# Kernel tuning notes

Hardware: AMD Instinct MI355X
Metric: run time of the kernel (lower is better)

Reference implementation:

```python
import jax, jax.numpy as jnp
import numpy as np

B, T_PLUS_2, H, K = 128, 2050, 64, 100
BETA = 1.0


def setup_inputs() -> dict:
    key = jax.random.key(0)
    ks = jax.random.split(key, 7)
    event_tensor = jax.random.randint(ks[0], (B, T_PLUS_2), 0, K)            # fine event types
    dtime_tensor = jax.random.uniform(ks[1], (B, T_PLUS_2), dtype=jnp.float32)
    scale = 1.0 / np.sqrt(H)
    in_emb = jax.random.normal(ks[2], (K + 3, H), dtype=jnp.float32) * scale  # +BOS/EOS/PAD rows
    Wx = jax.random.normal(ks[3], (H, 7 * H), dtype=jnp.float32) * scale      # input -> 7 gates
    Wh = jax.random.normal(ks[4], (H, 7 * H), dtype=jnp.float32) * scale      # hidden -> 7 gates
    b = jnp.zeros((7 * H,), dtype=jnp.float32)
    out_emb = jax.random.normal(ks[5], (K, H), dtype=jnp.float32) * scale     # coarse-type embeddings
    return {"event_tensor": event_tensor, "dtime_tensor": dtime_tensor,
            "in_emb": in_emb, "Wx": Wx, "Wh": Wh, "b": b, "out_emb": out_emb}


def _ctlstm_intensities(event_tensor, dtime_tensor, in_emb, Wx, Wh, b, out_emb):
    # Embed input events for steps 0..T (drop last token): [B, T+1, H]
    emb = in_emb[event_tensor[:, :-1]]
    # Precompute the input-dependent part of all 7 gates outside the scan.
    pre = jnp.einsum('bth,hg->btg', emb, Wx) + b        # [B, T+1, 7H]
    dt = dtime_tensor[:, 1:]                            # [B, T+1] dtime to next event

    batch = event_tensor.shape[0]
    h_dim = in_emb.shape[1]
    init = (jnp.zeros((batch, h_dim), jnp.float32),     # c(t_i-)
            jnp.zeros((batch, h_dim), jnp.float32),     # cell_bar
            jnp.zeros((batch, h_dim), jnp.float32))     # h(t_i-)

    def step(carry, inp):
        c_minus, cb_prev, h_minus = carry
        pre_t, dt_t = inp                               # [B,7H], [B]
        g = pre_t + h_minus @ Wh
        gi, gf, gz, go, gib, gfb, gd = jnp.split(g, 7, axis=-1)
        i = jax.nn.sigmoid(gi)
        f = jax.nn.sigmoid(gf)
        z = jnp.tanh(gz)
        o = jax.nn.sigmoid(go)
        i_bar = jax.nn.sigmoid(gib)
        f_bar = jax.nn.sigmoid(gfb)
        delta = jax.nn.softplus(gd)
        c_i = f * c_minus + i * z
        cb_i = f_bar * cb_prev + i_bar * z
        # decay over the interval dt: c(t)=cb+(c-cb)exp(-delta dt), h=o*tanh(c)
        c_next = cb_i + (c_i - cb_i) * jnp.exp(-delta * dt_t[:, None])
        h_next = o * jnp.tanh(c_next)
        return (c_next, cb_i, h_next), h_next

    _, hs = jax.lax.scan(step, init, (pre.transpose(1, 0, 2), dt.T))
    hs = hs.transpose(1, 0, 2)                          # [B, T+1, H] hidden at t_{i+1}^-
    # softplus with beta: (1/beta) * softplus(beta * x); identity fine<->coarse map
    logits = jnp.einsum('bth,kh->btk', hs, out_emb)
    return jax.nn.softplus(BETA * logits) / BETA        # [B, T+1, K]


def reference(event_tensor, dtime_tensor, in_emb, Wx, Wh, b, out_emb):
    return _ctlstm_intensities(event_tensor, dtime_tensor, in_emb, Wx, Wh, b, out_emb)
```

## Files before the change

kernel.cpp:

```cpp
#include <hip/hip_runtime.h>
#include <math.h>

#define BB 128
#define T2 2050
#define TT 2049
#define HH 64
#define GG 448
#define KK 100
#define NE 103

#define LOG2E 1.44269504088896340736f
#define LN2   0.69314718055994530942f

typedef short bf16x8 __attribute__((ext_vector_type(8)));
typedef float f32x4  __attribute__((ext_vector_type(4)));

__device__ __forceinline__ float frcp(float x) { return __builtin_amdgcn_rcpf(x); }

__device__ __forceinline__ float sigmoid_fast(float x) {
    return frcp(1.f + exp2f(-x * LOG2E));
}
__device__ __forceinline__ float tanh_fast(float x) {
    float e = exp2f(x * (2.f * LOG2E));
    return 1.f - 2.f * frcp(1.f + e);
}
__device__ __forceinline__ float softplus_fast(float x) {
    float t = exp2f(-fabsf(x) * LOG2E);
    return fmaxf(x, 0.f) + LN2 * log2f(1.f + t);
}

__device__ __forceinline__ unsigned short bf16_rne(float f) {
    unsigned int u = __builtin_bit_cast(unsigned int, f);
    unsigned int r = u + 0x7FFFu + ((u >> 16) & 1u);
    return (unsigned short)(r >> 16);
}
__device__ __forceinline__ float bf16_to_f(unsigned short s) {
    unsigned int u = ((unsigned int)s) << 16;
    return __builtin_bit_cast(float, u);
}

__global__ void pre_emb_kernel(const float* __restrict__ in_emb,
                               const float* __restrict__ Wx,
                               const float* __restrict__ bias,
                               float* __restrict__ pre_emb) {
    int e = blockIdx.x;
    int t = threadIdx.x;
    float acc = bias[t];
#pragma unroll
    for (int k = 0; k < HH; ++k)
        acc = fmaf(in_emb[e * HH + k], Wx[k * GG + t], acc);
    pre_emb[e * GG + t] = acc;
}

__device__ __forceinline__ void step_barrier() {
    __builtin_amdgcn_sched_barrier(0);
    asm volatile("s_waitcnt lgkmcnt(0)" ::: "memory");
    __builtin_amdgcn_s_barrier();
    __builtin_amdgcn_sched_barrier(0);
}

__launch_bounds__(512, 1)
__global__ void scan_kernel(const int* __restrict__ event,
                            const float* __restrict__ dtime,
                            const float* __restrict__ pre_emb,
                            const float* __restrict__ Wh,
                            const float* __restrict__ oe,
                            float* __restrict__ out) {
    const int b   = blockIdx.x;
    const int tid = threadIdx.x;
    const int w   = tid >> 6;
    const int l   = tid & 63;
    const int q   = l >> 4;
    const int m   = l & 15;

    __shared__ __align__(16) unsigned short hs_hi[2][HH];
    __shared__ __align__(16) unsigned short hs_lo[2][HH];

    const bool is_mat = (w < 4);
    const int  e      = ((w & 3) << 4) | m;

    const int*   ev_row  = event + b * T2;
    const float* dt_row  = dtime + b * T2;
    float*       out_row = out + (size_t)b * TT * KK;

    const f32x4 Z = { 0.f, 0.f, 0.f, 0.f };

    bf16x8 Bhi[7][2], Blo[7][2];
    bf16x8 Phi[2][2], Plo[2][2];
    const int jw  = w - 4;
    const int G0  = 2 * jw;
    const bool has1 = (2 * jw + 1) < 7;
    const int G1  = has1 ? (2 * jw + 1) : G0;

    if (is_mat) {
#pragma unroll
        for (int g = 0; g < 7; ++g) {
#pragma unroll
            for (int kh = 0; kh < 2; ++kh) {
                const int col = g * 64 + e;
                bf16x8 bh, bl;
#pragma unroll
                for (int j = 0; j < 8; ++j) {
                    const int k = kh * 32 + q * 8 + j;
                    const float v = Wh[k * GG + col];
                    const unsigned short hi = bf16_rne(v);
                    bh[j] = (short)hi;
                    bl[j] = (short)bf16_rne(v - bf16_to_f(hi));
                }
                Bhi[g][kh] = bh;
                Blo[g][kh] = bl;
            }
        }
    } else {
#pragma unroll
        for (int s = 0; s < 2; ++s) {
            const int Gs  = s ? G1 : G0;
            int col = Gs * 16 + m;
            if (col > KK - 1) col = KK - 1;
#pragma unroll
            for (int kh = 0; kh < 2; ++kh) {
                bf16x8 bh, bl;
#pragma unroll
                for (int j = 0; j < 8; ++j) {
                    const int k = kh * 32 + q * 8 + j;
                    const float v = oe[col * HH + k];
                    const unsigned short hi = bf16_rne(v);
                    bh[j] = (short)hi;
                    bl[j] = (short)bf16_rne(v - bf16_to_f(hi));
                }
                Phi[s][kh] = bh;
                Plo[s][kh] = bl;
            }
        }
    }

    float pre_cur[7];
    int   evn    = 0;
    float dt_cur = 0.f;
    float c = 0.f, cb = 0.f;
    if (is_mat) {
        const int ev0 = __builtin_amdgcn_readfirstlane(ev_row[0]);
        const float* pb0 = pre_emb + ev0 * GG;
#pragma unroll
        for (int g = 0; g < 7; ++g) pre_cur[g] = pb0[g * 64 + e];
        evn    = __builtin_amdgcn_readfirstlane(ev_row[1]);
        dt_cur = dt_row[1];
    }

    if (tid < HH) { hs_hi[0][tid] = 0; hs_lo[0][tid] = 0; }
    __syncthreads();

    constexpr int GORD[7] = { 6, 2, 0, 1, 4, 5, 3 };

    for (int t = 0; t < TT; ++t) {
        const int rb = t & 1;
        if (is_mat) {
            const float* pb = pre_emb + evn * GG;
            float pre_nxt[7];
#pragma unroll
            for (int g = 0; g < 7; ++g) pre_nxt[g] = pb[g * 64 + e];
            int t2 = t + 2; if (t2 > T2 - 1) t2 = T2 - 1;
            const int   ev_new = __builtin_amdgcn_readfirstlane(ev_row[t2]);
            const float dt_nxt = dt_row[t2];

            const bf16x8 Ahi0 = *(const bf16x8*)&hs_hi[rb][q * 8];
            const bf16x8 Ahi1 = *(const bf16x8*)&hs_hi[rb][32 + q * 8];
            const bf16x8 Alo0 = *(const bf16x8*)&hs_lo[rb][q * 8];
            const bf16x8 Alo1 = *(const bf16x8*)&hs_lo[rb][32 + q * 8];

            float gate[7];
#pragma unroll
            for (int gg = 0; gg < 7; ++gg) {
                const int g = GORD[gg];
                f32x4 aP = __builtin_amdgcn_mfma_f32_16x16x32_bf16(Ahi0, Bhi[g][0], Z, 0, 0, 0);
                f32x4 aQ = __builtin_amdgcn_mfma_f32_16x16x32_bf16(Ahi1, Bhi[g][1], Z, 0, 0, 0);
                aP = __builtin_amdgcn_mfma_f32_16x16x32_bf16(Alo0, Bhi[g][0], aP, 0, 0, 0);
                aQ = __builtin_amdgcn_mfma_f32_16x16x32_bf16(Alo1, Bhi[g][1], aQ, 0, 0, 0);
                aP = __builtin_amdgcn_mfma_f32_16x16x32_bf16(Ahi0, Blo[g][0], aP, 0, 0, 0);
                aQ = __builtin_amdgcn_mfma_f32_16x16x32_bf16(Ahi1, Blo[g][1], aQ, 0, 0, 0);
                gate[g] = pre_cur[g] + (aP[0] + aQ[0]);
            }

            const float ed   = exp2f(-dt_cur * log2f(1.f + exp2f(gate[6] * LOG2E)));
            const float z_g  = tanh_fast(gate[2]);
            const float i_g  = sigmoid_fast(gate[0]);
            const float f_g  = sigmoid_fast(gate[1]);
            const float ib_g = sigmoid_fast(gate[4]);
            const float fb_g = sigmoid_fast(gate[5]);
            const float o_g  = sigmoid_fast(gate[3]);

            const float ci  = fmaf(f_g, c, i_g * z_g);
            const float cbi = fmaf(fb_g, cb, ib_g * z_g);
            const float cn  = fmaf(ci - cbi, ed, cbi);
            const float h   = o_g * tanh_fast(cn);
            c  = cn;
            cb = cbi;

            const unsigned short hhi = bf16_rne(h);
            const unsigned short hlo = bf16_rne(h - bf16_to_f(hhi));
            const int wb = (t + 1) & 1;
            if (l < 32) {
                unsigned short* p = (l < 16) ? &hs_hi[wb][e] : &hs_lo[wb][e];
                *p = (l < 16) ? hhi : hlo;
            }

#pragma unroll
            for (int g = 0; g < 7; ++g) pre_cur[g] = pre_nxt[g];
            evn    = ev_new;
            dt_cur = dt_nxt;
        } else if (t > 0) {
            const bf16x8 Ahi0 = *(const bf16x8*)&hs_hi[rb][q * 8];
            const bf16x8 Ahi1 = *(const bf16x8*)&hs_hi[rb][32 + q * 8];
            const bf16x8 Alo0 = *(const bf16x8*)&hs_lo[rb][q * 8];
            const bf16x8 Alo1 = *(const bf16x8*)&hs_lo[rb][32 + q * 8];

            float lg[2];
#pragma unroll
            for (int s = 0; s < 2; ++s) {
                f32x4 aP = __builtin_amdgcn_mfma_f32_16x16x32_bf16(Ahi0, Phi[s][0], Z, 0, 0, 0);
                f32x4 aQ = __builtin_amdgcn_mfma_f32_16x16x32_bf16(Ahi1, Phi[s][1], Z, 0, 0, 0);
                aP = __builtin_amdgcn_mfma_f32_16x16x32_bf16(Alo0, Phi[s][0], aP, 0, 0, 0);
                aQ = __builtin_amdgcn_mfma_f32_16x16x32_bf16(Alo1, Phi[s][1], aQ, 0, 0, 0);
                aP = __builtin_amdgcn_mfma_f32_16x16x32_bf16(Ahi0, Plo[s][0], aP, 0, 0, 0);
                aQ = __builtin_amdgcn_mfma_f32_16x16x32_bf16(Ahi1, Plo[s][1], aQ, 0, 0, 0);
                lg[s] = aP[0] + aQ[0];
            }
            if (q == 0) {
                const int col0 = G0 * 16 + m;
                if (col0 < KK)
                    out_row[(size_t)(t - 1) * KK + col0] = softplus_fast(lg[0]);
                const int col1 = G1 * 16 + m;
                if (has1 && col1 < KK)
                    out_row[(size_t)(t - 1) * KK + col1] = softplus_fast(lg[1]);
            }
        }
        step_barrier();
    }

    if (!is_mat) {
        const int rb = TT & 1;
        const bf16x8 Ahi0 = *(const bf16x8*)&hs_hi[rb][q * 8];
        const bf16x8 Ahi1 = *(const bf16x8*)&hs_hi[rb][32 + q * 8];
        const bf16x8 Alo0 = *(const bf16x8*)&hs_lo[rb][q * 8];
        const bf16x8 Alo1 = *(const bf16x8*)&hs_lo[rb][32 + q * 8];

        float lg[2];
#pragma unroll
        for (int s = 0; s < 2; ++s) {
            f32x4 aP = __builtin_amdgcn_mfma_f32_16x16x32_bf16(Ahi0, Phi[s][0], Z, 0, 0, 0);
            f32x4 aQ = __builtin_amdgcn_mfma_f32_16x16x32_bf16(Ahi1, Phi[s][1], Z, 0, 0, 0);
            aP = __builtin_amdgcn_mfma_f32_16x16x32_bf16(Alo0, Phi[s][0], aP, 0, 0, 0);
            aQ = __builtin_amdgcn_mfma_f32_16x16x32_bf16(Alo1, Phi[s][1], aQ, 0, 0, 0);
            aP = __builtin_amdgcn_mfma_f32_16x16x32_bf16(Ahi0, Plo[s][0], aP, 0, 0, 0);
            aQ = __builtin_amdgcn_mfma_f32_16x16x32_bf16(Ahi1, Plo[s][1], aQ, 0, 0, 0);
            lg[s] = aP[0] + aQ[0];
        }
        if (q == 0) {
            const int col0 = G0 * 16 + m;
            if (col0 < KK)
                out_row[(size_t)(TT - 1) * KK + col0] = softplus_fast(lg[0]);
            const int col1 = G1 * 16 + m;
            if (has1 && col1 < KK)
                out_row[(size_t)(TT - 1) * KK + col1] = softplus_fast(lg[1]);
        }
    }
}

extern "C" void kernel_launch(void* const* d_in, const int* in_sizes, int n_in,
                              void* d_out, int out_size, void* d_ws, size_t ws_size,
                              hipStream_t stream) {
    const int*   event  = (const int*)d_in[0];
    const float* dtime  = (const float*)d_in[1];
    const float* in_emb = (const float*)d_in[2];
    const float* Wx     = (const float*)d_in[3];
    const float* Wh     = (const float*)d_in[4];
    const float* bias   = (const float*)d_in[5];
    const float* oe     = (const float*)d_in[6];
    float*       out    = (float*)d_out;

    float* pre_emb = (float*)d_ws;

    pre_emb_kernel<<<NE, GG, 0, stream>>>(in_emb, Wx, bias, pre_emb);
    scan_kernel<<<BB, 512, 0, stream>>>(event, dtime, pre_emb, Wh, oe, out);
}
```

Baseline: 1.739 ms.

## Stage event offsets and dtimes in LDS, unroll scan by two, raise matrix-wave priority

All event offsets and dtimes for the sequence are preloaded into shared memory before the scan. The per-step global loads of event/dt, which sat on the serial recurrence path, become LDS reads. The time loop is unrolled by two with even/odd prefetch buffers that prefetch the pre-gate vectors two steps ahead, and fixed double-buffer indices. The matrix waves get raised scheduling priority with s_setprio. This adds about 16KB of LDS and more registers.

```diff
diff --git a/kernel.cpp b/kernel.cpp
--- a/kernel.cpp
+++ b/kernel.cpp
@@ -8,6 +8,7 @@
 #define GG 448
 #define KK 100
 #define NE 103
+#define NSTAGE 2056
 
 #define LOG2E 1.44269504088896340736f
 #define LN2   0.69314718055994530942f
@@ -75,6 +76,8 @@
 
     __shared__ __align__(16) unsigned short hs_hi[2][HH];
     __shared__ __align__(16) unsigned short hs_lo[2][HH];
+    __shared__ int   evoff_s[NSTAGE];
+    __shared__ float dtl_s[NSTAGE];
 
     const bool is_mat = (w < 4);
     const int  e      = ((w & 3) << 4) | m;
@@ -84,13 +87,20 @@
     float*       out_row = out + (size_t)b * TT * KK;
 
     const f32x4 Z = { 0.f, 0.f, 0.f, 0.f };
+    constexpr int GORD[7] = { 6, 2, 0, 1, 4, 5, 3 };
+
+    for (int i = tid; i < NSTAGE; i += 512) {
+        const int idx = (i < T2) ? i : (T2 - 1);
+        evoff_s[i] = ev_row[idx] * GG;
+        dtl_s[i]   = dt_row[idx];
+    }
 
     bf16x8 Bhi[7][2], Blo[7][2];
     bf16x8 Phi[2][2], Plo[2][2];
-    const int jw  = w - 4;
-    const int G0  = 2 * jw;
+    const int jw    = w - 4;
+    const int G0    = 2 * jw;
     const bool has1 = (2 * jw + 1) < 7;
-    const int G1  = has1 ? (2 * jw + 1) : G0;
+    const int G1    = has1 ? (2 * jw + 1) : G0;
 
     if (is_mat) {
 #pragma unroll
@@ -114,7 +124,7 @@
     } else {
 #pragma unroll
         for (int s = 0; s < 2; ++s) {
-            const int Gs  = s ? G1 : G0;
+            const int Gs = s ? G1 : G0;
             int col = Gs * 16 + m;
             if (col > KK - 1) col = KK - 1;
 #pragma unroll
@@ -134,136 +144,122 @@
         }
     }
 
-    float pre_cur[7];
-    int   evn    = 0;
-    float dt_cur = 0.f;
-    float c = 0.f, cb = 0.f;
-    if (is_mat) {
-        const int ev0 = __builtin_amdgcn_readfirstlane(ev_row[0]);
-        const float* pb0 = pre_emb + ev0 * GG;
-#pragma unroll
-        for (int g = 0; g < 7; ++g) pre_cur[g] = pb0[g * 64 + e];
-        evn    = __builtin_amdgcn_readfirstlane(ev_row[1]);
-        dt_cur = dt_row[1];
-    }
-
     if (tid < HH) { hs_hi[0][tid] = 0; hs_lo[0][tid] = 0; }
     __syncthreads();
 
-    constexpr int GORD[7] = { 6, 2, 0, 1, 4, 5, 3 };
-
-    for (int t = 0; t < TT; ++t) {
-        const int rb = t & 1;
-        if (is_mat) {
-            const float* pb = pre_emb + evn * GG;
-            float pre_nxt[7];
-#pragma unroll
-            for (int g = 0; g < 7; ++g) pre_nxt[g] = pb[g * 64 + e];
-            int t2 = t + 2; if (t2 > T2 - 1) t2 = T2 - 1;
-            const int   ev_new = __builtin_amdgcn_readfirstlane(ev_row[t2]);
-            const float dt_nxt = dt_row[t2];
-
-            const bf16x8 Ahi0 = *(const bf16x8*)&hs_hi[rb][q * 8];
-            const bf16x8 Ahi1 = *(const bf16x8*)&hs_hi[rb][32 + q * 8];
-            const bf16x8 Alo0 = *(const bf16x8*)&hs_lo[rb][q * 8];
-            const bf16x8 Alo1 = *(const bf16x8*)&hs_lo[rb][32 + q * 8];
-
-            float gate[7];
-#pragma unroll
-            for (int gg = 0; gg < 7; ++gg) {
-                const int g = GORD[gg];
-                f32x4 aP = __builtin_amdgcn_mfma_f32_16x16x32_bf16(Ahi0, Bhi[g][0], Z, 0, 0, 0);
-                f32x4 aQ = __builtin_amdgcn_mfma_f32_16x16x32_bf16(Ahi1, Bhi[g][1], Z, 0, 0, 0);
-                aP = __builtin_amdgcn_mfma_f32_16x16x32_bf16(Alo0, Bhi[g][0], aP, 0, 0, 0);
-                aQ = __builtin_amdgcn_mfma_f32_16x16x32_bf16(Alo1, Bhi[g][1], aQ, 0, 0, 0);
-                aP = __builtin_amdgcn_mfma_f32_16x16x32_bf16(Ahi0, Blo[g][0], aP, 0, 0, 0);
-                aQ = __builtin_amdgcn_mfma_f32_16x16x32_bf16(Ahi1, Blo[g][1], aQ, 0, 0, 0);
-                gate[g] = pre_cur[g] + (aP[0] + aQ[0]);
-            }
-
-            const float ed   = exp2f(-dt_cur * log2f(1.f + exp2f(gate[6] * LOG2E)));
-            const float z_g  = tanh_fast(gate[2]);
-            const float i_g  = sigmoid_fast(gate[0]);
-            const float f_g  = sigmoid_fast(gate[1]);
-            const float ib_g = sigmoid_fast(gate[4]);
-            const float fb_g = sigmoid_fast(gate[5]);
-            const float o_g  = sigmoid_fast(gate[3]);
-
-            const float ci  = fmaf(f_g, c, i_g * z_g);
-            const float cbi = fmaf(fb_g, cb, ib_g * z_g);
-            const float cn  = fmaf(ci - cbi, ed, cbi);
-            const float h   = o_g * tanh_fast(cn);
-            c  = cn;
-            cb = cbi;
-
-            const unsigned short hhi = bf16_rne(h);
-            const unsigned short hlo = bf16_rne(h - bf16_to_f(hhi));
-            const int wb = (t + 1) & 1;
-            if (l < 32) {
-                unsigned short* p = (l < 16) ? &hs_hi[wb][e] : &hs_lo[wb][e];
-                *p = (l < 16) ? hhi : hlo;
-            }
-
-#pragma unroll
-            for (int g = 0; g < 7; ++g) pre_cur[g] = pre_nxt[g];
-            evn    = ev_new;
-            dt_cur = dt_nxt;
-        } else if (t > 0) {
-            const bf16x8 Ahi0 = *(const bf16x8*)&hs_hi[rb][q * 8];
-            const bf16x8 Ahi1 = *(const bf16x8*)&hs_hi[rb][32 + q * 8];
-            const bf16x8 Alo0 = *(const bf16x8*)&hs_lo[rb][q * 8];
-            const bf16x8 Alo1 = *(const bf16x8*)&hs_lo[rb][32 + q * 8];
-
-            float lg[2];
-#pragma unroll
-            for (int s = 0; s < 2; ++s) {
-                f32x4 aP = __builtin_amdgcn_mfma_f32_16x16x32_bf16(Ahi0, Phi[s][0], Z, 0, 0, 0);
-                f32x4 aQ = __builtin_amdgcn_mfma_f32_16x16x32_bf16(Ahi1, Phi[s][1], Z, 0, 0, 0);
-                aP = __builtin_amdgcn_mfma_f32_16x16x32_bf16(Alo0, Phi[s][0], aP, 0, 0, 0);
-                aQ = __builtin_amdgcn_mfma_f32_16x16x32_bf16(Alo1, Phi[s][1], aQ, 0, 0, 0);
-                aP = __builtin_amdgcn_mfma_f32_16x16x32_bf16(Ahi0, Plo[s][0], aP, 0, 0, 0);
-                aQ = __builtin_amdgcn_mfma_f32_16x16x32_bf16(Ahi1, Plo[s][1], aQ, 0, 0, 0);
-                lg[s] = aP[0] + aQ[0];
-            }
-            if (q == 0) {
-                const int col0 = G0 * 16 + m;
-                if (col0 < KK)
-                    out_row[(size_t)(t - 1) * KK + col0] = softplus_fast(lg[0]);
-                const int col1 = G1 * 16 + m;
-                if (has1 && col1 < KK)
-                    out_row[(size_t)(t - 1) * KK + col1] = softplus_fast(lg[1]);
-            }
+    float preE[7], preO[7];
+    int   offE = 0, offO = 0;
+    float dtE = 0.f, dtO = 0.f;
+    if (is_mat) {
+        const int o0 = evoff_s[0], o1 = evoff_s[1];
+#pragma unroll
+        for (int g = 0; g < 7; ++g) {
+            preE[g] = pre_emb[o0 + g * 64 + e];
+            preO[g] = pre_emb[o1 + g * 64 + e];
         }
+        offE = evoff_s[2];
+        offO = evoff_s[3];
+        dtE  = dtl_s[1];
+        dtO  = dtl_s[2];
+    }
+
+    const int  col0   = G0 * 16 + m;
+    const int  col1   = G1 * 16 + m;
+    const bool c0ok   = (col0 < KK);
+    const bool c1ok   = has1 && (col1 < KK);
+    float*     outP   = out_row;
+
+#define MAT_STEP(RB, WB, PRE, OFF, DTV, TIDX)                                   \
+    {                                                                           \
+        float pc[7];                                                            \
+        _Pragma("unroll") for (int g = 0; g < 7; ++g) pc[g] = PRE[g];           \
+        const float* pb = pre_emb + OFF;                                        \
+        _Pragma("unroll") for (int g = 0; g < 7; ++g) PRE[g] = pb[g * 64 + e];  \
+        OFF = evoff_s[(TIDX) + 4];                                              \
+        const float dtc = DTV;                                                  \
+        DTV = dtl_s[(TIDX) + 3];                                                \
+        const bf16x8 Ahi0 = *(const bf16x8*)&hs_hi[RB][q * 8];                  \
+        const bf16x8 Ahi1 = *(const bf16x8*)&hs_hi[RB][32 + q * 8];             \
+        const bf16x8 Alo0 = *(const bf16x8*)&hs_lo[RB][q * 8];                  \
+        const bf16x8 Alo1 = *(const bf16x8*)&hs_lo[RB][32 + q * 8];             \
+        float gate[7];                                                          \
+        _Pragma("unroll") for (int gg = 0; gg < 7; ++gg) {                      \
+            const int g = GORD[gg];                                             \
+            f32x4 aP = __builtin_amdgcn_mfma_f32_16x16x32_bf16(Ahi0, Bhi[g][0], Z, 0, 0, 0); \
+            f32x4 aQ = __builtin_amdgcn_mfma_f32_16x16x32_bf16(Ahi1, Bhi[g][1], Z, 0, 0, 0); \
+            aP = __builtin_amdgcn_mfma_f32_16x16x32_bf16(Alo0, Bhi[g][0], aP, 0, 0, 0); \
+            aQ = __builtin_amdgcn_mfma_f32_16x16x32_bf16(Alo1, Bhi[g][1], aQ, 0, 0, 0); \
+            aP = __builtin_amdgcn_mfma_f32_16x16x32_bf16(Ahi0, Blo[g][0], aP, 0, 0, 0); \
+            aQ = __builtin_amdgcn_mfma_f32_16x16x32_bf16(Ahi1, Blo[g][1], aQ, 0, 0, 0); \
+            gate[g] = pc[g] + (aP[0] + aQ[0]);                                  \
+        }                                                                       \
+        const float ed   = exp2f(-dtc * log2f(1.f + exp2f(gate[6] * LOG2E)));   \
+        const float z_g  = tanh_fast(gate[2]);                                  \
+        const float i_g  = sigmoid_fast(gate[0]);                               \
+        const float f_g  = sigmoid_fast(gate[1]);                               \
+        const float ib_g = sigmoid_fast(gate[4]);                               \
+        const float fb_g = sigmoid_fast(gate[5]);                               \
+        const float o_g  = sigmoid_fast(gate[3]);                               \
+        const float ci  = fmaf(f_g, c, i_g * z_g);                              \
+        const float cbi = fmaf(fb_g, cb, ib_g * z_g);                           \
+        const float cn  = fmaf(ci - cbi, ed, cbi);                              \
+        const float h   = o_g * tanh_fast(cn);                                  \
+        c  = cn;                                                                \
+        cb = cbi;                                                               \
+        const unsigned short hhi = bf16_rne(h);                                 \
+        const unsigned short hlo = bf16_rne(h - bf16_to_f(hhi));                \
+        if (l < 32) {                                                           \
+            unsigned short* p = (l < 16) ? &hs_hi[WB][e] : &hs_lo[WB][e];       \
+            *p = (l < 16) ? hhi : hlo;                                          \
+        }                                                                       \
+    }
+
+#define LOGIT_STEP(RB, DO_STORE)                                                \
+    {                                                                           \
+        const bf16x8 Ahi0 = *(const bf16x8*)&hs_hi[RB][q * 8];                  \
+        const bf16x8 Ahi1 = *(const bf16x8*)&hs_hi[RB][32 + q * 8];             \
+        const bf16x8 Alo0 = *(const bf16x8*)&hs_lo[RB][q * 8];                  \
+        const bf16x8 Alo1 = *(const bf16x8*)&hs_lo[RB][32 + q * 8];             \
+        float lg[2];                                                            \
+        _Pragma("unroll") for (int s = 0; s < 2; ++s) {                         \
+            f32x4 aP = __builtin_amdgcn_mfma_f32_16x16x32_bf16(Ahi0, Phi[s][0], Z, 0, 0, 0); \
+            f32x4 aQ = __builtin_amdgcn_mfma_f32_16x16x32_bf16(Ahi1, Phi[s][1], Z, 0, 0, 0); \
+            aP = __builtin_amdgcn_mfma_f32_16x16x32_bf16(Alo0, Phi[s][0], aP, 0, 0, 0); \
+            aQ = __builtin_amdgcn_mfma_f32_16x16x32_bf16(Alo1, Phi[s][1], aQ, 0, 0, 0); \
+            aP = __builtin_amdgcn_mfma_f32_16x16x32_bf16(Ahi0, Plo[s][0], aP, 0, 0, 0); \
+            aQ = __builtin_amdgcn_mfma_f32_16x16x32_bf16(Ahi1, Plo[s][1], aQ, 0, 0, 0); \
+            lg[s] = aP[0] + aQ[0];                                              \
+        }                                                                       \
+        if (DO_STORE) {                                                         \
+            if (q == 0) {                                                       \
+                if (c0ok) outP[col0] = softplus_fast(lg[0]);                    \
+                if (c1ok) outP[col1] = softplus_fast(lg[1]);                    \
+            }                                                                   \
+            outP += KK;                                                         \
+        }                                                                       \
+    }
+
+    float c = 0.f, cb = 0.f;
+    if (is_mat) __builtin_amdgcn_s_setprio(1);
+
+    for (int tp = 0; tp < (TT - 1) / 2; ++tp) {
+        const int te = 2 * tp;
+        if (is_mat) { MAT_STEP(0, 1, preE, offE, dtE, te) }
+        else        { LOGIT_STEP(0, (tp > 0)) }
         step_barrier();
-    }
-
-    if (!is_mat) {
-        const int rb = TT & 1;
-        const bf16x8 Ahi0 = *(const bf16x8*)&hs_hi[rb][q * 8];
-        const bf16x8 Ahi1 = *(const bf16x8*)&hs_hi[rb][32 + q * 8];
-        const bf16x8 Alo0 = *(const bf16x8*)&hs_lo[rb][q * 8];
-        const bf16x8 Alo1 = *(const bf16x8*)&hs_lo[rb][32 + q * 8];
-
-        float lg[2];
-#pragma unroll
-        for (int s = 0; s < 2; ++s) {
-            f32x4 aP = __builtin_amdgcn_mfma_f32_16x16x32_bf16(Ahi0, Phi[s][0], Z, 0, 0, 0);
-            f32x4 aQ = __builtin_amdgcn_mfma_f32_16x16x32_bf16(Ahi1, Phi[s][1], Z, 0, 0, 0);
-            aP = __builtin_amdgcn_mfma_f32_16x16x32_bf16(Alo0, Phi[s][0], aP, 0, 0, 0);
-            aQ = __builtin_amdgcn_mfma_f32_16x16x32_bf16(Alo1, Phi[s][1], aQ, 0, 0, 0);
-            aP = __builtin_amdgcn_mfma_f32_16x16x32_bf16(Ahi0, Plo[s][0], aP, 0, 0, 0);
-            aQ = __builtin_amdgcn_mfma_f32_16x16x32_bf16(Ahi1, Plo[s][1], aQ, 0, 0, 0);
-            lg[s] = aP[0] + aQ[0];
-        }
-        if (q == 0) {
-            const int col0 = G0 * 16 + m;
-            if (col0 < KK)
-                out_row[(size_t)(TT - 1) * KK + col0] = softplus_fast(lg[0]);
-            const int col1 = G1 * 16 + m;
-            if (has1 && col1 < KK)
-                out_row[(size_t)(TT - 1) * KK + col1] = softplus_fast(lg[1]);
-        }
-    }
+        if (is_mat) { MAT_STEP(1, 0, preO, offO, dtO, te + 1) }
+        else        { LOGIT_STEP(1, true) }
+        step_barrier();
+    }
+    if (is_mat) { MAT_STEP(0, 1, preE, offE, dtE, TT - 1) }
+    else        { LOGIT_STEP(0, true) }
+    step_barrier();
+    if (is_mat) __builtin_amdgcn_s_setprio(0);
+
+    if (!is_mat) { LOGIT_STEP(1, true) }
+
+#undef MAT_STEP
+#undef LOGIT_STEP
 }
 
 extern "C" void kernel_launch(void* const* d_in, const int* in_sizes, int n_in,
```

Result: faster. 1.680 ms (-3.4%).
